# Kernel optimization log

Measured on AMD Instinct MI355X. Metric: run time of the kernel, lower is better.

Reference implementation:

```python
import jax, jax.numpy as jnp
import numpy as np

N = 100000
E = 1600000
F = 128
HID = 64
OUT = 64
LSTM_H = (3 * HID) // 2  # 96, PyG JumpingKnowledge lstm hidden size


def setup_inputs() -> dict:
    key = jax.random.key(0)
    ks = jax.random.split(key, 40)

    def w(k, shape, s=0.05):
        return jax.random.normal(k, shape, dtype=jnp.float32) * s

    inp = {}
    inp['x'] = jax.random.normal(ks[0], (N, F), dtype=jnp.float32)
    inp['edge_index'] = jax.random.randint(ks[1], (2, E), 0, N)
    # GINConv MLPs: Linear(in,hid) -> ReLU -> Linear(hid,hid)
    dims = [(F, HID), (HID, HID), (HID, HID)]
    for i, (a, b) in enumerate(dims):
        inp[f'W{i}a'] = w(ks[2 + 4 * i], (b, a))
        inp[f'b{i}a'] = w(ks[3 + 4 * i], (b,))
        inp[f'W{i}b'] = w(ks[4 + 4 * i], (b, b))
        inp[f'b{i}b'] = w(ks[5 + 4 * i], (b,))
    # JK bidirectional LSTM (torch gate order i,f,g,o)
    for j, d in enumerate(['f', 'b']):
        inp[f'Wih_{d}'] = w(ks[14 + 4 * j], (4 * LSTM_H, HID))
        inp[f'Whh_{d}'] = w(ks[15 + 4 * j], (4 * LSTM_H, LSTM_H))
        inp[f'bih_{d}'] = w(ks[16 + 4 * j], (4 * LSTM_H,))
        inp[f'bhh_{d}'] = w(ks[17 + 4 * j], (4 * LSTM_H,))
    inp['Watt'] = w(ks[22], (1, 2 * LSTM_H))
    inp['batt'] = w(ks[23], (1,))
    inp['Wlin'] = w(ks[24], (OUT, HID))
    inp['blin'] = w(ks[25], (OUT,))
    inp['Wfc1'] = w(ks[26], (1, OUT))
    inp['bfc1'] = w(ks[27], (1,))
    inp['Wfc2'] = w(ks[28], (1, N))
    inp['bfc2'] = w(ks[29], (1,))
    return inp


def _gin_layer(h, src, dst, Wa, ba, Wb, bb):
    # GINConv with eps=0: MLP((1+eps)*x + sum_{j in N(i)} x_j)
    agg = jax.ops.segment_sum(h[src], dst, num_segments=h.shape[0])
    z = h + agg
    z = jnp.maximum(z @ Wa.T + ba, 0.0)
    return z @ Wb.T + bb


def _lstm_scan(seq, Wih, Whh, bih, bhh):
    # seq: [L, N, C]; returns hidden states [L, N, H]
    H = Whh.shape[1]
    bias = bih + bhh

    def cell(carry, xt):
        hp, cp = carry
        g = xt @ Wih.T + hp @ Whh.T + bias
        i, f, gg, o = jnp.split(g, 4, axis=-1)
        c = jax.nn.sigmoid(f) * cp + jax.nn.sigmoid(i) * jnp.tanh(gg)
        hn = jax.nn.sigmoid(o) * jnp.tanh(c)
        return (hn, c), hn

    n = seq.shape[1]
    init = (jnp.zeros((n, H), seq.dtype), jnp.zeros((n, H), seq.dtype))
    _, hs = jax.lax.scan(cell, init, seq)
    return hs


def reference(x, edge_index, W0a, b0a, W0b, b0b, W1a, b1a, W1b, b1b,
              W2a, b2a, W2b, b2b, Wih_f, Whh_f, bih_f, bhh_f,
              Wih_b, Whh_b, bih_b, bhh_b, Watt, batt, Wlin, blin,
              Wfc1, bfc1, Wfc2, bfc2):
    src, dst = edge_index[0], edge_index[1]
    h = x
    xs = []
    for (Wa, ba, Wb, bb) in [(W0a, b0a, W0b, b0b), (W1a, b1a, W1b, b1b),
                             (W2a, b2a, W2b, b2b)]:
        h = _gin_layer(h, src, dst, Wa, ba, Wb, bb)
        h = jnp.maximum(h, 0.0)  # BasicGNN act (relu); dropout=identity in eval
        xs.append(h)
    seq = jnp.stack(xs, axis=0)  # [L, N, HID]
    hf = _lstm_scan(seq, Wih_f, Whh_f, bih_f, bhh_f)
    hb = _lstm_scan(seq[::-1], Wih_b, Whh_b, bih_b, bhh_b)[::-1]
    ao = jnp.concatenate([hf, hb], axis=-1)  # [L, N, 2*LSTM_H]
    alpha = (ao @ Watt.T + batt)[..., 0]  # [L, N]
    alpha = jax.nn.softmax(alpha, axis=0)  # softmax over layers
    xjk = jnp.einsum('lnc,ln->nc', seq, alpha)  # [N, HID]
    xo = xjk @ Wlin.T + blin  # [N, OUT]
    v = (xo @ Wfc1.T + bfc1)[:, 0]  # [N]
    v = jnp.where(v >= 0, v, 0.01 * v)  # LeakyReLU
    return Wfc2 @ v + bfc2  # [1]
```

## Files before the change

kernel.cpp:

```cpp
#include <hip/hip_runtime.h>
#include <stdint.h>

typedef unsigned short u16;
typedef unsigned int u32;
using short8 = __attribute__((ext_vector_type(8))) short;
using f32x16 = __attribute__((ext_vector_type(16))) float;

__device__ __forceinline__ float sigf(float x){
  return __builtin_amdgcn_rcpf(1.0f + __expf(-x));
}
__device__ __forceinline__ float tanh_f(float x){
  return 1.0f - 2.0f*__builtin_amdgcn_rcpf(1.0f + __expf(2.0f*x));
}
__device__ __forceinline__ u16 f2bf(float f){
  u32 u = __float_as_uint(f);
  u += 0x7FFFu + ((u>>16)&1u);
  return (u16)(u>>16);
}
__device__ __forceinline__ float bf2f(u16 h){ return __uint_as_float(((u32)h)<<16); }

__global__ void k_deg(const int* __restrict__ dst, int* __restrict__ deg, int E){
  int i = blockIdx.x*256 + threadIdx.x;
  if (i < E) atomicAdd(&deg[dst[i]], 1);
}

__global__ __launch_bounds__(256) void k_scan1(const int* __restrict__ deg, int* __restrict__ indptr,
                                               int* __restrict__ bsum, int N){
  __shared__ int s[256];
  int tid = threadIdx.x;
  int i = blockIdx.x*256 + tid;
  int v = (i < N) ? deg[i] : 0;
  s[tid] = v; __syncthreads();
  for (int off=1; off<256; off<<=1){
    int t = (tid>=off) ? s[tid-off] : 0;
    __syncthreads();
    s[tid] += t;
    __syncthreads();
  }
  if (i < N) indptr[i] = s[tid] - v;
  if (tid == 255) bsum[blockIdx.x] = s[255];
}

__global__ __launch_bounds__(512) void k_scan2(const int* __restrict__ bsum, int* __restrict__ boffs,
                                               int* __restrict__ indptr, int nb, int N){
  __shared__ int s[512];
  int tid = threadIdx.x;
  int v = (tid < nb) ? bsum[tid] : 0;
  s[tid] = v; __syncthreads();
  for (int off=1; off<512; off<<=1){
    int t = (tid>=off) ? s[tid-off] : 0;
    __syncthreads();
    s[tid] += t;
    __syncthreads();
  }
  boffs[tid] = s[tid] - v;
  if (tid == nb-1) indptr[N] = s[tid];
}

__global__ __launch_bounds__(256) void k_scan3(int* __restrict__ indptr, const int* __restrict__ boffs, int N){
  int i = blockIdx.x*256 + threadIdx.x;
  if (i < N) indptr[i] += boffs[blockIdx.x];
}

__global__ void k_fill(const int* __restrict__ src, const int* __restrict__ dst,
                       const int* __restrict__ indptr, int* __restrict__ fill,
                       int* __restrict__ col, int E){
  int i = blockIdx.x*256 + threadIdx.x;
  if (i < E){
    int d = dst[i];
    int r = atomicAdd(&fill[d], 1);
    col[indptr[d] + r] = src[i];
  }
}

template<int F>
__global__ __launch_bounds__(256) void k_agg(const float* __restrict__ y, const int* __restrict__ indptr,
                                             const int* __restrict__ col, const float* __restrict__ bias,
                                             float* __restrict__ z, int N){
  constexpr int TPN = F/4;
  constexpr int NPB = 256/TPN;
  int n = blockIdx.x*NPB + threadIdx.x/TPN;
  int lane = threadIdx.x % TPN;
  if (n >= N) return;
  const float4* hv = (const float4*)y;
  float4 acc = hv[(size_t)n*TPN + lane];
  int s = indptr[n], e = indptr[n+1];
  int p = s;
  for (; p + 8 <= e; p += 8){
    int c8[8];
    #pragma unroll
    for (int i=0;i<8;++i) c8[i] = col[p+i];
    #pragma unroll
    for (int i=0;i<8;++i){
      float4 x = hv[(size_t)c8[i]*TPN + lane];
      acc.x += x.x; acc.y += x.y; acc.z += x.z; acc.w += x.w;
    }
  }
  for (; p < e; ++p){
    float4 x = hv[(size_t)col[p]*TPN + lane];
    acc.x += x.x; acc.y += x.y; acc.z += x.z; acc.w += x.w;
  }
  float4 b4 = ((const float4*)bias)[lane];
  acc.x = fmaxf(acc.x + b4.x, 0.f);
  acc.y = fmaxf(acc.y + b4.y, 0.f);
  acc.z = fmaxf(acc.z + b4.z, 0.f);
  acc.w = fmaxf(acc.w + b4.w, 0.f);
  ((float4*)z)[(size_t)n*TPN + lane] = acc;
}

__global__ __launch_bounds__(256) void k_packG(const float* __restrict__ W, u16* __restrict__ Wg, int K){
  int idx = blockIdx.x*256 + threadIdx.x;
  if (idx >= K*128) return;
  int i  = idx & 7;
  int l  = (idx>>3) & 63;
  int p  = (idx>>9) & 1;
  int rt = (idx>>10) & 1;
  int kt = idx >> 11;
  int j  = rt*32 + (l & 31);
  int k  = kt*16 + ((l>>5)<<3) + i;
  float v = W[(size_t)j*K + k];
  u16 h = f2bf(v);
  Wg[idx] = p ? f2bf(v - bf2f(h)) : h;
}

__device__ __forceinline__ void cvt8p(const float (&v)[8], u32 (&hw)[4], u32 (&lw)[4]){
  #pragma unroll
  for (int i=0;i<4;++i){
    u16 h0=f2bf(v[2*i]),   h1=f2bf(v[2*i+1]);
    u16 l0=f2bf(v[2*i]-bf2f(h0)), l1=f2bf(v[2*i+1]-bf2f(h1));
    hw[i]= (u32)h0 | ((u32)h1<<16);
    lw[i]= (u32)l0 | ((u32)l1<<16);
  }
}

template<int K, int ACT>
__global__ __launch_bounds__(256,2) void k_mfgemm(const float* __restrict__ A, const u16* __restrict__ Wg,
                                                  const float* __restrict__ bias, float* __restrict__ out,
                                                  int N){
  constexpr int NKT = K/16;
  __shared__ u16 BH[2*NKT*512];
  __shared__ u16 BL[2*NKT*512];
  const int tid = threadIdx.x;
  const int l = tid & 63;
  const int w = __builtin_amdgcn_readfirstlane(tid >> 6);
  const int rt = w >> 1, nt = w & 1;
  const int nb = blockIdx.x * 64;
  const int hi = l >> 5;

  for (int u = tid; u < 64*(K/8); u += 256){
    int node = u / (K/8);
    int kc = u % (K/8);
    int n = nb + node;
    float v[8];
    if (n < N){
      const float4* s4 = (const float4*)(A + (size_t)n*K + kc*8);
      float4 a = s4[0], b = s4[1];
      v[0]=a.x; v[1]=a.y; v[2]=a.z; v[3]=a.w; v[4]=b.x; v[5]=b.y; v[6]=b.z; v[7]=b.w;
    } else {
      #pragma unroll
      for (int i=0;i<8;++i) v[i]=0.f;
    }
    u32 hw[4], lw[4];
    cvt8p(v, hw, lw);
    int kt = kc >> 1, h2 = kc & 1;
    int sl = (((h2<<5) | (node&31)) ^ (kc & 7));
    int addr = (((node>>5)*NKT + kt)<<9) + (sl<<3);
    *(uint4*)(BH + addr) = make_uint4(hw[0],hw[1],hw[2],hw[3]);
    *(uint4*)(BL + addr) = make_uint4(lw[0],lw[1],lw[2],lw[3]);
  }
  __syncthreads();

  f32x16 acc;
  #pragma unroll
  for (int r=0;r<16;++r) acc[r] = 0.f;
  const u16* wbase = Wg + ((size_t)rt<<10) + ((size_t)l<<3);
  #pragma unroll
  for (int kt = 0; kt < NKT; ++kt){
    const u16* wk = wbase + (size_t)kt*2048;
    short8 Ah = *(const short8*)(wk);
    short8 Al = *(const short8*)(wk + 512);
    int sl = l ^ (((kt<<1) + hi) & 7);
    int baddr = ((nt*NKT + kt)<<9) + (sl<<3);
    short8 Bh = *(const short8*)(BH + baddr);
    short8 Bl = *(const short8*)(BL + baddr);
    acc = __builtin_amdgcn_mfma_f32_32x32x16_bf16(Ah, Bh, acc, 0,0,0);
    acc = __builtin_amdgcn_mfma_f32_32x32x16_bf16(Ah, Bl, acc, 0,0,0);
    acc = __builtin_amdgcn_mfma_f32_32x32x16_bf16(Al, Bh, acc, 0,0,0);
  }

  const int col = l & 31;
  const int n = nb + nt*32 + col;
  if (n < N){
    #pragma unroll
    for (int g = 0; g < 4; ++g){
      const int j0 = rt*32 + 8*g + 4*hi;
      float4 b4 = bias ? *(const float4*)(bias + j0) : make_float4(0.f,0.f,0.f,0.f);
      float4 o;
      o.x = acc[4*g+0] + b4.x;
      o.y = acc[4*g+1] + b4.y;
      o.z = acc[4*g+2] + b4.z;
      o.w = acc[4*g+3] + b4.w;
      if (ACT){
        o.x = fmaxf(o.x, 0.f); o.y = fmaxf(o.y, 0.f);
        o.z = fmaxf(o.z, 0.f); o.w = fmaxf(o.w, 0.f);
      }
      *(float4*)(out + (size_t)n*64 + j0) = o;
    }
  }
}

__global__ __launch_bounds__(256) void k_packW1(const float* __restrict__ Wih, const float* __restrict__ Whh,
                                                u16* __restrict__ Wp){
  int idx = blockIdx.x*256 + threadIdx.x;
  if (idx >= 10*12*64*8) return;
  int i  = idx & 7;
  int l  = (idx>>3) & 63;
  int rt = (idx>>9) % 12;
  int kt = (idx>>9) / 12;
  int r  = rt*32 + (l & 31);
  int j  = r >> 2, g = r & 3;
  int row = g*96 + j;
  int k  = kt*16 + ((l>>5)<<3) + i;
  float v = (k < 64) ? Wih[row*64 + k] : Whh[row*96 + (k-64)];
  Wp[idx] = f2bf(v);
}

__global__ __launch_bounds__(128) void k_packB(const float* __restrict__ bih, const float* __restrict__ bhh,
                                               float4* __restrict__ Bp){
  int j = blockIdx.x*128 + threadIdx.x;
  if (j >= 96) return;
  Bp[j] = make_float4(bih[j]+bhh[j], bih[96+j]+bhh[96+j],
                      bih[192+j]+bhh[192+j], bih[288+j]+bhh[288+j]);
}

__device__ __forceinline__ void ldx_regs(const float* __restrict__ seq, int blk, int N, int tid,
                                         float (&v)[8]){
  int node = tid >> 3;
  int kc = tid & 7;
  int n = blk*32 + node;
  if (n < N){
    const float4* s4 = (const float4*)(seq + (size_t)n*64 + kc*8);
    float4 a = s4[0], b = s4[1];
    v[0]=a.x; v[1]=a.y; v[2]=a.z; v[3]=a.w; v[4]=b.x; v[5]=b.y; v[6]=b.z; v[7]=b.w;
  } else {
    #pragma unroll
    for (int i=0;i<8;++i) v[i]=0.f;
  }
}

__device__ __forceinline__ void stage_from_regs(const float (&v)[8], u16* __restrict__ XH,
                                                u16* __restrict__ XL, int tid){
  int node = tid >> 3;
  int kc = tid & 7;
  u32 hw[4], lw[4];
  cvt8p(v, hw, lw);
  int kt = kc >> 1, hi = kc & 1;
  int sl = (((hi<<5) | node) ^ (kc & 7));
  int addr = (kt<<9) + (sl<<3);
  *(uint4*)(XH + addr) = make_uint4(hw[0],hw[1],hw[2],hw[3]);
  *(uint4*)(XL + addr) = make_uint4(lw[0],lw[1],lw[2],lw[3]);
}

__device__ __forceinline__ void restage_h(const float (*hF)[32], u16* __restrict__ XH,
                                          u16* __restrict__ XL, int tid){
  int node = tid & 31;
  #pragma unroll
  for (int q = 0; q < 2; ++q){
    int cc = (tid >> 5) + q*8;
    if (cc < 12){
      int kth = cc >> 1, hi = cc & 1;
      int ktG = kth + 4;
      float v[8];
      #pragma unroll
      for (int i=0;i<8;++i) v[i] = hF[cc*8 + i][node];
      u32 hw[4], lw[4];
      cvt8p(v, hw, lw);
      int sl = (((hi<<5) | node) ^ ((2*ktG + hi) & 7));
      int addr = (ktG<<9) + (sl<<3);
      *(uint4*)(XH + addr) = make_uint4(hw[0],hw[1],hw[2],hw[3]);
      *(uint4*)(XL + addr) = make_uint4(lw[0],lw[1],lw[2],lw[3]);
    }
  }
}

template<int FIRST, int WRITEH>
__device__ __forceinline__ float lstm_step5(const u16* __restrict__ Wp,
    const float4* __restrict__ Bp, const float* __restrict__ WattW,
    const u16* __restrict__ XH, const u16* __restrict__ XL, float (*hF)[32],
    float (&c)[12], int rtg, int l)
{
  constexpr int NKT = FIRST ? 4 : 10;
  const int hi = l >> 5;
  const int col = l & 31;
  f32x16 acc[3];
  #pragma unroll
  for (int t=0;t<3;++t)
    #pragma unroll
    for (int r=0;r<16;++r) acc[t][r] = 0.f;

  const u16* wbase = Wp + (size_t)(rtg*3)*512 + ((size_t)l<<3);
  #pragma unroll
  for (int kt = 0; kt < NKT; ++kt){
    const u16* wk = wbase + (size_t)kt*6144;
    short8 A0 = *(const short8*)(wk);
    short8 A1 = *(const short8*)(wk + 512);
    short8 A2 = *(const short8*)(wk + 1024);
    int sl = l ^ (((kt<<1) + hi) & 7);
    int baddr = (kt<<9) + (sl<<3);
    short8 Bh = *(const short8*)(XH + baddr);
    short8 Bl = *(const short8*)(XL + baddr);
    __builtin_amdgcn_s_setprio(1);
    acc[0] = __builtin_amdgcn_mfma_f32_32x32x16_bf16(A0, Bh, acc[0], 0,0,0);
    acc[1] = __builtin_amdgcn_mfma_f32_32x32x16_bf16(A1, Bh, acc[1], 0,0,0);
    acc[2] = __builtin_amdgcn_mfma_f32_32x32x16_bf16(A2, Bh, acc[2], 0,0,0);
    acc[0] = __builtin_amdgcn_mfma_f32_32x32x16_bf16(A0, Bl, acc[0], 0,0,0);
    acc[1] = __builtin_amdgcn_mfma_f32_32x32x16_bf16(A1, Bl, acc[1], 0,0,0);
    acc[2] = __builtin_amdgcn_mfma_f32_32x32x16_bf16(A2, Bl, acc[2], 0,0,0);
    __builtin_amdgcn_s_setprio(0);
  }

  float aP = 0.f;
  #pragma unroll
  for (int ti=0;ti<3;++ti){
    #pragma unroll
    for (int rg=0; rg<4; ++rg){
      const int j = (rtg*3+ti)*8 + 2*rg + hi;
      float4 bv = Bp[j];
      float gi = acc[ti][rg*4+0] + bv.x;
      float gf = acc[ti][rg*4+1] + bv.y;
      float gg = acc[ti][rg*4+2] + bv.z;
      float go = acc[ti][rg*4+3] + bv.w;
      const int ci = ti*4 + rg;
      float cp = FIRST ? 0.f : c[ci];
      float cn = sigf(gf)*cp + sigf(gi)*tanh_f(gg);
      float hh = sigf(go)*tanh_f(cn);
      c[ci] = cn;
      aP = fmaf(hh, WattW[j], aP);
      if (WRITEH) hF[j][col] = hh;
    }
  }
  return aP;
}

__global__ __launch_bounds__(256,2) void k_lstm5(
    const float* __restrict__ h1, const float* __restrict__ h2, const float* __restrict__ h3,
    const u16* __restrict__ Wpf, const u16* __restrict__ Wpb,
    const float4* __restrict__ Bpf, const float4* __restrict__ Bpb,
    const float* __restrict__ Watt, const float* __restrict__ batt,
    float* __restrict__ aF, float* __restrict__ aB, int gL, int N)
{
  __shared__ u16 XH[5120];
  __shared__ u16 XL[5120];
  __shared__ float hF[96][32];
  __shared__ float sAl[4][3][32];
  const int tid = threadIdx.x;
  const int l = tid & 63;
  const int rtg = __builtin_amdgcn_readfirstlane(tid >> 6);
  const int dir = (blockIdx.x >= gL) ? 1 : 0;
  const int blk = blockIdx.x - dir*gL;
  const float* sA = dir ? h3 : h1;
  const float* sC = dir ? h1 : h3;
  const u16* Wp = dir ? Wpb : Wpf;
  const float4* Bp = dir ? Bpb : Bpf;
  const float* WattW = Watt + dir*96;
  float* aD = dir ? aB : aF;
  float c[12];
  float a0, a1, a2;
  float xv[8];

  ldx_regs(sA, blk, N, tid, xv);
  stage_from_regs(xv, XH, XL, tid);
  ldx_regs(h2, blk, N, tid, xv);
  __syncthreads();

  a0 = lstm_step5<1,1>(Wp, Bp, WattW, XH, XL, hF, c, rtg, l);
  __syncthreads();
  stage_from_regs(xv, XH, XL, tid);
  restage_h(hF, XH, XL, tid);
  ldx_regs(sC, blk, N, tid, xv);
  __syncthreads();

  a1 = lstm_step5<0,1>(Wp, Bp, WattW, XH, XL, hF, c, rtg, l);
  __syncthreads();
  stage_from_regs(xv, XH, XL, tid);
  restage_h(hF, XH, XL, tid);
  __syncthreads();

  a2 = lstm_step5<0,0>(Wp, Bp, WattW, XH, XL, hF, c, rtg, l);

  a0 += __shfl_xor(a0, 32);
  a1 += __shfl_xor(a1, 32);
  a2 += __shfl_xor(a2, 32);
  if (l < 32){
    sAl[rtg][0][l] = a0;
    sAl[rtg][1][l] = a1;
    sAl[rtg][2][l] = a2;
  }
  __syncthreads();
  if (tid < 96){
    int s = tid >> 5;
    int node = tid & 31;
    int n = blk*32 + node;
    if (n < N){
      float sum = sAl[0][s][node] + sAl[1][s][node]
                + sAl[2][s][node] + sAl[3][s][node];
      int slice = dir ? (2 - s) : s;
      float v = dir ? sum : (batt[0] + sum);
      aD[(size_t)slice*N + n] = v;
    }
  }
}

__global__ __launch_bounds__(256) void k_jk(const float* __restrict__ aF, const float* __restrict__ aB,
                                            const float* __restrict__ h1, const float* __restrict__ h2,
                                            const float* __restrict__ h3,
                                            const float* __restrict__ Wlin, const float* __restrict__ blin,
                                            const float* __restrict__ Wfc1, const float* __restrict__ bfc1,
                                            float* __restrict__ vout, int N){
  __shared__ float sWl[64*65];
  __shared__ float sX[4][64];
  int tid = threadIdx.x;
  for (int idx = tid; idx < 1024; idx += 256){
    int j = idx >> 4;
    int c4 = (idx & 15) << 2;
    float4 v = *(const float4*)(Wlin + (size_t)j*64 + c4);
    sWl[j*65 + c4+0] = v.x; sWl[j*65 + c4+1] = v.y;
    sWl[j*65 + c4+2] = v.z; sWl[j*65 + c4+3] = v.w;
  }
  __syncthreads();
  int ln = tid >> 6, j = tid & 63;
  float wf1 = Wfc1[j];
  float bl = blin[j];
  for (int ib = 0; ib < 4; ++ib){
    int n = blockIdx.x*16 + ib*4 + ln;
    bool ok = n < N;
    float xj = 0.f;
    if (ok){
      float a0 = aF[n] + aB[n];
      float a1 = aF[(size_t)N + n] + aB[(size_t)N + n];
      float a2 = aF[(size_t)2*N + n] + aB[(size_t)2*N + n];
      float m = fmaxf(a0, fmaxf(a1, a2));
      float e0 = __expf(a0-m), e1 = __expf(a1-m), e2 = __expf(a2-m);
      float inv = __builtin_amdgcn_rcpf(e0+e1+e2);
      float w0 = e0*inv, w1 = e1*inv, w2 = e2*inv;
      xj = w0*h1[(size_t)n*64 + j] + w1*h2[(size_t)n*64 + j] + w2*h3[(size_t)n*64 + j];
    }
    sX[ln][j] = xj;
    __syncthreads();
    float acc = bl;
    #pragma unroll 8
    for (int cc = 0; cc < 64; ++cc) acc = fmaf(sX[ln][cc], sWl[j*65 + cc], acc);
    float r = acc * wf1;
    #pragma unroll
    for (int off = 32; off > 0; off >>= 1) r += __shfl_down(r, off);
    if (j == 0 && ok){
      float vv = r + bfc1[0];
      vout[n] = vv >= 0.f ? vv : 0.01f*vv;
    }
    __syncthreads();
  }
}

__global__ __launch_bounds__(256) void k_final1(const float* __restrict__ w, const float* __restrict__ v,
                                                double* __restrict__ part, int N){
  __shared__ double sd[256];
  int tid = threadIdx.x;
  double a = 0.0;
  for (int i = blockIdx.x*256 + tid; i < N; i += 256*256)
    a += (double)(w[i] * v[i]);
  sd[tid] = a; __syncthreads();
  for (int off = 128; off > 0; off >>= 1){
    if (tid < off) sd[tid] += sd[tid + off];
    __syncthreads();
  }
  if (tid == 0) part[blockIdx.x] = sd[0];
}

__global__ __launch_bounds__(256) void k_final2(const double* __restrict__ part, const float* __restrict__ bfc2,
                                                float* __restrict__ out){
  __shared__ double sd[256];
  int tid = threadIdx.x;
  sd[tid] = part[tid]; __syncthreads();
  for (int off = 128; off > 0; off >>= 1){
    if (tid < off) sd[tid] += sd[tid + off];
    __syncthreads();
  }
  if (tid == 0) out[0] = (float)(sd[0] + (double)bfc2[0]);
}

extern "C" void kernel_launch(void* const* d_in, const int* in_sizes, int n_in,
                              void* d_out, int out_size, void* d_ws, size_t ws_size,
                              hipStream_t stream){
  const float* x    = (const float*)d_in[0];
  const int*   ei   = (const int*)d_in[1];
  const float* W0a  = (const float*)d_in[2];
  const float* b0a  = (const float*)d_in[3];
  const float* W0b  = (const float*)d_in[4];
  const float* b0b  = (const float*)d_in[5];
  const float* W1a  = (const float*)d_in[6];
  const float* b1a  = (const float*)d_in[7];
  const float* W1b  = (const float*)d_in[8];
  const float* b1b  = (const float*)d_in[9];
  const float* W2a  = (const float*)d_in[10];
  const float* b2a  = (const float*)d_in[11];
  const float* W2b  = (const float*)d_in[12];
  const float* b2b  = (const float*)d_in[13];
  const float* Wih_f = (const float*)d_in[14];
  const float* Whh_f = (const float*)d_in[15];
  const float* bih_f = (const float*)d_in[16];
  const float* bhh_f = (const float*)d_in[17];
  const float* Wih_b = (const float*)d_in[18];
  const float* Whh_b = (const float*)d_in[19];
  const float* bih_b = (const float*)d_in[20];
  const float* bhh_b = (const float*)d_in[21];
  const float* Watt = (const float*)d_in[22];
  const float* batt = (const float*)d_in[23];
  const float* Wlin = (const float*)d_in[24];
  const float* blin = (const float*)d_in[25];
  const float* Wfc1 = (const float*)d_in[26];
  const float* bfc1 = (const float*)d_in[27];
  const float* Wfc2 = (const float*)d_in[28];
  const float* bfc2 = (const float*)d_in[29];
  float* out = (float*)d_out;

  const int N = in_sizes[0] / 128;
  const int E = in_sizes[1] / 2;
  const int* src = ei;
  const int* dst = ei + E;

  uint8_t* w8 = (uint8_t*)d_ws;
  size_t off = 0;
  auto alloc = [&](size_t bytes) -> void* {
    void* p = w8 + off;
    off = (off + bytes + 255) & ~(size_t)255;
    return p;
  };
  int*    deg    = (int*)   alloc((size_t)N*4);
  int*    fill   = (int*)   alloc((size_t)N*4);
  int*    indptr = (int*)   alloc(((size_t)N+1)*4);
  int*    col    = (int*)   alloc((size_t)E*4);
  int*    bsum   = (int*)   alloc(2048);
  int*    boffs  = (int*)   alloc(2048);
  float*  h1     = (float*) alloc((size_t)N*64*4);
  float*  h2     = (float*) alloc((size_t)N*64*4);
  float*  h3     = (float*) alloc((size_t)N*64*4);
  float*  aF     = (float*) alloc((size_t)3*N*4);
  float*  aB     = (float*) alloc((size_t)3*N*4);
  float*  vbuf   = (float*) alloc((size_t)N*4);
  double* part   = (double*)alloc(256*8);
  u16*    Wpf    = (u16*)   alloc((size_t)10*12*64*8*2);
  u16*    Wpb    = (u16*)   alloc((size_t)10*12*64*8*2);
  float4* Bpf    = (float4*)alloc((size_t)96*16);
  float4* Bpb    = (float4*)alloc((size_t)96*16);
  u16*    Wg0a   = (u16*)   alloc((size_t)128*128*2);
  u16*    Wg0b   = (u16*)   alloc((size_t)64*128*2);
  u16*    Wg1a   = (u16*)   alloc((size_t)64*128*2);
  u16*    Wg1b   = (u16*)   alloc((size_t)64*128*2);
  u16*    Wg2a   = (u16*)   alloc((size_t)64*128*2);
  u16*    Wg2b   = (u16*)   alloc((size_t)64*128*2);
  float*  P      = (float*) alloc((size_t)N*192*4);
  if (off > ws_size) return;
  float* ybuf = P;
  float* zbuf = P + (size_t)N*64;

  hipMemsetAsync(deg,  0, (size_t)N*4, stream);
  hipMemsetAsync(fill, 0, (size_t)N*4, stream);

  int gE = (E + 255) / 256;
  int nb1 = (N + 255) / 256;
  int gG = (N + 63) / 64;
  int gA = (N + 15) / 16;
  int gL = (N + 31) / 32;

  k_packW1<<<240, 256, 0, stream>>>(Wih_f, Whh_f, Wpf);
  k_packW1<<<240, 256, 0, stream>>>(Wih_b, Whh_b, Wpb);
  k_packB<<<1, 128, 0, stream>>>(bih_f, bhh_f, Bpf);
  k_packB<<<1, 128, 0, stream>>>(bih_b, bhh_b, Bpb);
  k_packG<<<64, 256, 0, stream>>>(W0a, Wg0a, 128);
  k_packG<<<32, 256, 0, stream>>>(W0b, Wg0b, 64);
  k_packG<<<32, 256, 0, stream>>>(W1a, Wg1a, 64);
  k_packG<<<32, 256, 0, stream>>>(W1b, Wg1b, 64);
  k_packG<<<32, 256, 0, stream>>>(W2a, Wg2a, 64);
  k_packG<<<32, 256, 0, stream>>>(W2b, Wg2b, 64);

  k_deg  <<<gE, 256, 0, stream>>>(dst, deg, E);
  k_scan1<<<nb1, 256, 0, stream>>>(deg, indptr, bsum, N);
  k_scan2<<<1, 512, 0, stream>>>(bsum, boffs, indptr, nb1, N);
  k_scan3<<<nb1, 256, 0, stream>>>(indptr, boffs, N);
  k_fill <<<gE, 256, 0, stream>>>(src, dst, indptr, fill, col, E);

  k_mfgemm<128,0><<<gG, 256, 0, stream>>>(x, Wg0a, nullptr, ybuf, N);
  k_agg<64><<<gA, 256, 0, stream>>>(ybuf, indptr, col, b0a, zbuf, N);
  k_mfgemm<64,1><<<gG, 256, 0, stream>>>(zbuf, Wg0b, b0b, h1, N);
  k_mfgemm<64,0><<<gG, 256, 0, stream>>>(h1, Wg1a, nullptr, ybuf, N);
  k_agg<64><<<gA, 256, 0, stream>>>(ybuf, indptr, col, b1a, zbuf, N);
  k_mfgemm<64,1><<<gG, 256, 0, stream>>>(zbuf, Wg1b, b1b, h2, N);
  k_mfgemm<64,0><<<gG, 256, 0, stream>>>(h2, Wg2a, nullptr, ybuf, N);
  k_agg<64><<<gA, 256, 0, stream>>>(ybuf, indptr, col, b2a, zbuf, N);
  k_mfgemm<64,1><<<gG, 256, 0, stream>>>(zbuf, Wg2b, b2b, h3, N);

  k_lstm5<<<2*gL, 256, 0, stream>>>(h1, h2, h3, Wpf, Wpb, Bpf, Bpb, Watt, batt,
                                    aF, aB, gL, N);

  k_jk<<<gA, 256, 0, stream>>>(aF, aB, h1, h2, h3, Wlin, blin, Wfc1, bfc1, vbuf, N);

  k_final1<<<256, 256, 0, stream>>>(Wfc2, vbuf, part, N);
  k_final2<<<1, 256, 0, stream>>>(part, bfc2, out);
}
```

Before: 696.5 us.

## Fuse back-to-back GIN GEMMs and move JK linear onto split-bf16 MFMA

Adds k_mfgemm2, which computes layer L's second linear (bias+ReLU) and immediately feeds the result through shared memory into layer L+1's first linear. This removes one kernel launch and one re-read of h per layer. Also rewrites the JK stage as k_jk2, which stages the softmax-weighted mix into LDS and uses the 3-pass bf16 MFMA for Wlin, replacing the scalar FMA loop, then reduces with Wfc1 across lanes and waves. This adds LDS use (extra hX buffer) that may lower occupancy, and the split-bf16 path changes numerics slightly.

After: 660.9 us. 1.05x faster.

```diff
diff --git a/kernel.cpp b/kernel.cpp
--- a/kernel.cpp
+++ b/kernel.cpp
@@ -133,6 +133,17 @@
   }
 }
 
+__device__ __forceinline__ void stageG(const float (&v)[8], u16* __restrict__ BH, u16* __restrict__ BL,
+                                       int node, int kc, int NKT){
+  u32 hw[4], lw[4];
+  cvt8p(v, hw, lw);
+  int kt = kc >> 1, h2 = kc & 1;
+  int sl = (((h2<<5) | (node&31)) ^ (kc & 7));
+  int addr = (((node>>5)*NKT + kt)<<9) + (sl<<3);
+  *(uint4*)(BH + addr) = make_uint4(hw[0],hw[1],hw[2],hw[3]);
+  *(uint4*)(BL + addr) = make_uint4(lw[0],lw[1],lw[2],lw[3]);
+}
+
 template<int K, int ACT>
 __global__ __launch_bounds__(256,2) void k_mfgemm(const float* __restrict__ A, const u16* __restrict__ Wg,
                                                   const float* __restrict__ bias, float* __restrict__ out,
@@ -160,13 +171,7 @@
       #pragma unroll
       for (int i=0;i<8;++i) v[i]=0.f;
     }
-    u32 hw[4], lw[4];
-    cvt8p(v, hw, lw);
-    int kt = kc >> 1, h2 = kc & 1;
-    int sl = (((h2<<5) | (node&31)) ^ (kc & 7));
-    int addr = (((node>>5)*NKT + kt)<<9) + (sl<<3);
-    *(uint4*)(BH + addr) = make_uint4(hw[0],hw[1],hw[2],hw[3]);
-    *(uint4*)(BL + addr) = make_uint4(lw[0],lw[1],lw[2],lw[3]);
+    stageG(v, BH, BL, node, kc, NKT);
   }
   __syncthreads();
 
@@ -205,6 +210,114 @@
         o.z = fmaxf(o.z, 0.f); o.w = fmaxf(o.w, 0.f);
       }
       *(float4*)(out + (size_t)n*64 + j0) = o;
+    }
+  }
+}
+
+__global__ __launch_bounds__(256,2) void k_mfgemm2(const float* __restrict__ Z, const u16* __restrict__ Wgb,
+                                                   const float* __restrict__ bb, const u16* __restrict__ Wga,
+                                                   float* __restrict__ Hout, float* __restrict__ Yout,
+                                                   int N){
+  __shared__ u16 BH[4096];
+  __shared__ u16 BL[4096];
+  __shared__ float hX[64][68];
+  const int tid = threadIdx.x;
+  const int l = tid & 63;
+  const int w = __builtin_amdgcn_readfirstlane(tid >> 6);
+  const int rt = w >> 1, nt = w & 1;
+  const int nb = blockIdx.x * 64;
+  const int hi = l >> 5;
+  const int col = l & 31;
+  const int n = nb + nt*32 + col;
+
+  for (int u = tid; u < 512; u += 256){
+    int node = u >> 3;
+    int kc = u & 7;
+    int nn = nb + node;
+    float v[8];
+    if (nn < N){
+      const float4* s4 = (const float4*)(Z + (size_t)nn*64 + kc*8);
+      float4 a = s4[0], b = s4[1];
+      v[0]=a.x; v[1]=a.y; v[2]=a.z; v[3]=a.w; v[4]=b.x; v[5]=b.y; v[6]=b.z; v[7]=b.w;
+    } else {
+      #pragma unroll
+      for (int i=0;i<8;++i) v[i]=0.f;
+    }
+    stageG(v, BH, BL, node, kc, 4);
+  }
+  __syncthreads();
+
+  f32x16 acc;
+  #pragma unroll
+  for (int r=0;r<16;++r) acc[r] = 0.f;
+  {
+    const u16* wbase = Wgb + ((size_t)rt<<10) + ((size_t)l<<3);
+    #pragma unroll
+    for (int kt = 0; kt < 4; ++kt){
+      const u16* wk = wbase + (size_t)kt*2048;
+      short8 Ah = *(const short8*)(wk);
+      short8 Al = *(const short8*)(wk + 512);
+      int sl = l ^ (((kt<<1) + hi) & 7);
+      int baddr = ((nt*4 + kt)<<9) + (sl<<3);
+      short8 Bh = *(const short8*)(BH + baddr);
+      short8 Bl = *(const short8*)(BL + baddr);
+      acc = __builtin_amdgcn_mfma_f32_32x32x16_bf16(Ah, Bh, acc, 0,0,0);
+      acc = __builtin_amdgcn_mfma_f32_32x32x16_bf16(Ah, Bl, acc, 0,0,0);
+      acc = __builtin_amdgcn_mfma_f32_32x32x16_bf16(Al, Bh, acc, 0,0,0);
+    }
+  }
+  {
+    const int node = nt*32 + col;
+    #pragma unroll
+    for (int g = 0; g < 4; ++g){
+      const int j0 = rt*32 + 8*g + 4*hi;
+      float4 b4 = *(const float4*)(bb + j0);
+      float4 o;
+      o.x = fmaxf(acc[4*g+0] + b4.x, 0.f);
+      o.y = fmaxf(acc[4*g+1] + b4.y, 0.f);
+      o.z = fmaxf(acc[4*g+2] + b4.z, 0.f);
+      o.w = fmaxf(acc[4*g+3] + b4.w, 0.f);
+      if (n < N) *(float4*)(Hout + (size_t)n*64 + j0) = o;
+      *(float4*)(&hX[node][j0]) = o;
+    }
+  }
+  __syncthreads();
+
+  for (int u = tid; u < 512; u += 256){
+    int node = u >> 3;
+    int kc = u & 7;
+    float v[8];
+    #pragma unroll
+    for (int i=0;i<8;++i) v[i] = hX[node][kc*8 + i];
+    stageG(v, BH, BL, node, kc, 4);
+  }
+  __syncthreads();
+
+  #pragma unroll
+  for (int r=0;r<16;++r) acc[r] = 0.f;
+  {
+    const u16* wbase = Wga + ((size_t)rt<<10) + ((size_t)l<<3);
+    #pragma unroll
+    for (int kt = 0; kt < 4; ++kt){
+      const u16* wk = wbase + (size_t)kt*2048;
+      short8 Ah = *(const short8*)(wk);
+      short8 Al = *(const short8*)(wk + 512);
+      int sl = l ^ (((kt<<1) + hi) & 7);
+      int baddr = ((nt*4 + kt)<<9) + (sl<<3);
+      short8 Bh = *(const short8*)(BH + baddr);
+      short8 Bl = *(const short8*)(BL + baddr);
+      acc = __builtin_amdgcn_mfma_f32_32x32x16_bf16(Ah, Bh, acc, 0,0,0);
+      acc = __builtin_amdgcn_mfma_f32_32x32x16_bf16(Ah, Bl, acc, 0,0,0);
+      acc = __builtin_amdgcn_mfma_f32_32x32x16_bf16(Al, Bh, acc, 0,0,0);
+    }
+  }
+  if (n < N){
+    #pragma unroll
+    for (int g = 0; g < 4; ++g){
+      const int j0 = rt*32 + 8*g + 4*hi;
+      float4 o;
+      o.x = acc[4*g+0]; o.y = acc[4*g+1]; o.z = acc[4*g+2]; o.w = acc[4*g+3];
+      *(float4*)(Yout + (size_t)n*64 + j0) = o;
     }
   }
 }
@@ -411,31 +524,29 @@
   }
 }
 
-__global__ __launch_bounds__(256) void k_jk(const float* __restrict__ aF, const float* __restrict__ aB,
-                                            const float* __restrict__ h1, const float* __restrict__ h2,
-                                            const float* __restrict__ h3,
-                                            const float* __restrict__ Wlin, const float* __restrict__ blin,
-                                            const float* __restrict__ Wfc1, const float* __restrict__ bfc1,
-                                            float* __restrict__ vout, int N){
-  __shared__ float sWl[64*65];
-  __shared__ float sX[4][64];
-  int tid = threadIdx.x;
-  for (int idx = tid; idx < 1024; idx += 256){
-    int j = idx >> 4;
-    int c4 = (idx & 15) << 2;
-    float4 v = *(const float4*)(Wlin + (size_t)j*64 + c4);
-    sWl[j*65 + c4+0] = v.x; sWl[j*65 + c4+1] = v.y;
-    sWl[j*65 + c4+2] = v.z; sWl[j*65 + c4+3] = v.w;
-  }
-  __syncthreads();
-  int ln = tid >> 6, j = tid & 63;
-  float wf1 = Wfc1[j];
-  float bl = blin[j];
-  for (int ib = 0; ib < 4; ++ib){
-    int n = blockIdx.x*16 + ib*4 + ln;
-    bool ok = n < N;
-    float xj = 0.f;
-    if (ok){
+__global__ __launch_bounds__(256,2) void k_jk2(const float* __restrict__ aF, const float* __restrict__ aB,
+                                               const float* __restrict__ h1, const float* __restrict__ h2,
+                                               const float* __restrict__ h3,
+                                               const u16* __restrict__ WgL, const float* __restrict__ blin,
+                                               const float* __restrict__ Wfc1, const float* __restrict__ bfc1,
+                                               float* __restrict__ vout, int N){
+  __shared__ u16 BH[4096];
+  __shared__ u16 BL[4096];
+  __shared__ float sP[4][32];
+  const int tid = threadIdx.x;
+  const int l = tid & 63;
+  const int w = __builtin_amdgcn_readfirstlane(tid >> 6);
+  const int rt = w >> 1, nt = w & 1;
+  const int nb = blockIdx.x * 64;
+  const int hi = l >> 5;
+  const int col = l & 31;
+
+  for (int u = tid; u < 512; u += 256){
+    int node = u >> 3;
+    int kc = u & 7;
+    int n = nb + node;
+    float v[8];
+    if (n < N){
       float a0 = aF[n] + aB[n];
       float a1 = aF[(size_t)N + n] + aB[(size_t)N + n];
       float a2 = aF[(size_t)2*N + n] + aB[(size_t)2*N + n];
@@ -443,21 +554,63 @@
       float e0 = __expf(a0-m), e1 = __expf(a1-m), e2 = __expf(a2-m);
       float inv = __builtin_amdgcn_rcpf(e0+e1+e2);
       float w0 = e0*inv, w1 = e1*inv, w2 = e2*inv;
-      xj = w0*h1[(size_t)n*64 + j] + w1*h2[(size_t)n*64 + j] + w2*h3[(size_t)n*64 + j];
-    }
-    sX[ln][j] = xj;
-    __syncthreads();
-    float acc = bl;
-    #pragma unroll 8
-    for (int cc = 0; cc < 64; ++cc) acc = fmaf(sX[ln][cc], sWl[j*65 + cc], acc);
-    float r = acc * wf1;
-    #pragma unroll
-    for (int off = 32; off > 0; off >>= 1) r += __shfl_down(r, off);
-    if (j == 0 && ok){
-      float vv = r + bfc1[0];
-      vout[n] = vv >= 0.f ? vv : 0.01f*vv;
-    }
-    __syncthreads();
+      const float4* p1 = (const float4*)(h1 + (size_t)n*64 + kc*8);
+      const float4* p2 = (const float4*)(h2 + (size_t)n*64 + kc*8);
+      const float4* p3 = (const float4*)(h3 + (size_t)n*64 + kc*8);
+      #pragma unroll
+      for (int q=0;q<2;++q){
+        float4 x1 = p1[q], x2 = p2[q], x3 = p3[q];
+        v[4*q+0] = w0*x1.x + w1*x2.x + w2*x3.x;
+        v[4*q+1] = w0*x1.y + w1*x2.y + w2*x3.y;
+        v[4*q+2] = w0*x1.z + w1*x2.z + w2*x3.z;
+        v[4*q+3] = w0*x1.w + w1*x2.w + w2*x3.w;
+      }
+    } else {
+      #pragma unroll
+      for (int i=0;i<8;++i) v[i]=0.f;
+    }
+    stageG(v, BH, BL, node, kc, 4);
+  }
+  __syncthreads();
+
+  f32x16 acc;
+  #pragma unroll
+  for (int r=0;r<16;++r) acc[r] = 0.f;
+  const u16* wbase = WgL + ((size_t)rt<<10) + ((size_t)l<<3);
+  #pragma unroll
+  for (int kt = 0; kt < 4; ++kt){
+    const u16* wk = wbase + (size_t)kt*2048;
+    short8 Ah = *(const short8*)(wk);
+    short8 Al = *(const short8*)(wk + 512);
+    int sl = l ^ (((kt<<1) + hi) & 7);
+    int baddr = ((nt*4 + kt)<<9) + (sl<<3);
+    short8 Bh = *(const short8*)(BH + baddr);
+    short8 Bl = *(const short8*)(BL + baddr);
+    acc = __builtin_amdgcn_mfma_f32_32x32x16_bf16(Ah, Bh, acc, 0,0,0);
+    acc = __builtin_amdgcn_mfma_f32_32x32x16_bf16(Ah, Bl, acc, 0,0,0);
+    acc = __builtin_amdgcn_mfma_f32_32x32x16_bf16(Al, Bh, acc, 0,0,0);
+  }
+
+  float p = 0.f;
+  #pragma unroll
+  for (int g = 0; g < 4; ++g){
+    #pragma unroll
+    for (int rg = 0; rg < 4; ++rg){
+      const int j = rt*32 + 8*g + 4*hi + rg;
+      p += (acc[4*g+rg] + blin[j]) * Wfc1[j];
+    }
+  }
+  p += __shfl_xor(p, 32);
+  if (l < 32) sP[w][l] = p;
+  __syncthreads();
+  if (tid < 64){
+    int node = tid;
+    int nt2 = node >> 5, c2 = node & 31;
+    int n = nb + node;
+    if (n < N){
+      float t = sP[nt2][c2] + sP[2+nt2][c2] + bfc1[0];
+      vout[n] = t >= 0.f ? t : 0.01f*t;
+    }
   }
 }
 
@@ -558,6 +711,7 @@
   u16*    Wg1b   = (u16*)   alloc((size_t)64*128*2);
   u16*    Wg2a   = (u16*)   alloc((size_t)64*128*2);
   u16*    Wg2b   = (u16*)   alloc((size_t)64*128*2);
+  u16*    WgL    = (u16*)   alloc((size_t)64*128*2);
   float*  P      = (float*) alloc((size_t)N*192*4);
   if (off > ws_size) return;
   float* ybuf = P;
@@ -582,6 +736,7 @@
   k_packG<<<32, 256, 0, stream>>>(W1b, Wg1b, 64);
   k_packG<<<32, 256, 0, stream>>>(W2a, Wg2a, 64);
   k_packG<<<32, 256, 0, stream>>>(W2b, Wg2b, 64);
+  k_packG<<<32, 256, 0, stream>>>(Wlin, WgL, 64);
 
   k_deg  <<<gE, 256, 0, stream>>>(dst, deg, E);
   k_scan1<<<nb1, 256, 0, stream>>>(deg, indptr, bsum, N);
@@ -591,18 +746,16 @@
 
   k_mfgemm<128,0><<<gG, 256, 0, stream>>>(x, Wg0a, nullptr, ybuf, N);
   k_agg<64><<<gA, 256, 0, stream>>>(ybuf, indptr, col, b0a, zbuf, N);
-  k_mfgemm<64,1><<<gG, 256, 0, stream>>>(zbuf, Wg0b, b0b, h1, N);
-  k_mfgemm<64,0><<<gG, 256, 0, stream>>>(h1, Wg1a, nullptr, ybuf, N);
+  k_mfgemm2<<<gG, 256, 0, stream>>>(zbuf, Wg0b, b0b, Wg1a, h1, ybuf, N);
   k_agg<64><<<gA, 256, 0, stream>>>(ybuf, indptr, col, b1a, zbuf, N);
-  k_mfgemm<64,1><<<gG, 256, 0, stream>>>(zbuf, Wg1b, b1b, h2, N);
-  k_mfgemm<64,0><<<gG, 256, 0, stream>>>(h2, Wg2a, nullptr, ybuf, N);
+  k_mfgemm2<<<gG, 256, 0, stream>>>(zbuf, Wg1b, b1b, Wg2a, h2, ybuf, N);
   k_agg<64><<<gA, 256, 0, stream>>>(ybuf, indptr, col, b2a, zbuf, N);
   k_mfgemm<64,1><<<gG, 256, 0, stream>>>(zbuf, Wg2b, b2b, h3, N);
 
   k_lstm5<<<2*gL, 256, 0, stream>>>(h1, h2, h3, Wpf, Wpb, Bpf, Bpb, Watt, batt,
                                     aF, aB, gL, N);
 
-  k_jk<<<gA, 256, 0, stream>>>(aF, aB, h1, h2, h3, Wlin, blin, Wfc1, bfc1, vbuf, N);
+  k_jk2<<<gG, 256, 0, stream>>>(aF, aB, h1, h2, h3, WgL, blin, Wfc1, bfc1, vbuf, N);
 
   k_final1<<<256, 256, 0, stream>>>(Wfc2, vbuf, part, N);
   k_final2<<<1, 256, 0, stream>>>(part, bfc2, out);
```
